# Optimization experiments

Measured on AMD Instinct MI355X. Metric: run time of the kernel, lower is better.

The kernel has to match this reference:

```python
import jax, jax.numpy as jnp
import numpy as np

B, H, W, C = 32, 56, 56, 256
WS, SHIFT, HEADS = 7, 3, 8
HD = C // HEADS
HIDDEN = 4 * C
N = WS * WS
NW = (H // WS) * (W // WS)
EPS = 1e-5


def _rel_pos_indices():
    coords = np.stack(np.meshgrid(np.arange(WS), np.arange(WS), indexing='ij'), -1).reshape(-1, 2)
    rel = coords[None, :, :] - coords[:, None, :]
    rel[..., 0] += WS - 1
    rel[..., 1] += WS - 1
    rel[..., 0] *= 2 * WS - 1
    return rel.sum(-1)  # (N, N) int

_REL_IDX = jnp.asarray(_rel_pos_indices())


def _attn_mask():
    img = np.zeros((H, W), np.float32)
    sl = (slice(0, -WS), slice(-WS, -SHIFT), slice(-SHIFT, None))
    tag = 0
    for hs in sl:
        for ws_ in sl:
            img[hs, ws_] = tag
            tag += 1
    mw = img.reshape(H // WS, WS, W // WS, WS).transpose(0, 2, 1, 3).reshape(-1, N)
    diff = mw[:, None, :] - mw[:, :, None]
    return jnp.asarray(np.where(diff != 0, -100.0, 0.0).astype(np.float32))  # (NW, N, N)

_MASK = _attn_mask()


def _layernorm(x, g, b):
    mu = x.mean(-1, keepdims=True)
    var = ((x - mu) ** 2).mean(-1, keepdims=True)
    return (x - mu) * jax.lax.rsqrt(var + EPS) * g + b


def _win_partition(x):  # (B,H,W,C) -> (B*NW, N, C)
    x = x.reshape(B, H // WS, WS, W // WS, WS, C)
    return x.transpose(0, 1, 3, 2, 4, 5).reshape(-1, N, C)


def _win_reverse(w):  # (B*NW, N, C) -> (B,H,W,C)
    x = w.reshape(B, H // WS, W // WS, WS, WS, C)
    return x.transpose(0, 1, 3, 2, 4, 5).reshape(B, H, W, C)


def setup_inputs() -> dict:
    key = jax.random.key(0)
    ks = jax.random.split(key, 16)
    s = 0.02
    return {
        'x': jax.random.normal(ks[0], (B, H * W, C), jnp.float32),
        'norm1_g': jnp.ones((C,), jnp.float32),
        'norm1_b': jnp.zeros((C,), jnp.float32),
        'qkv_w': jax.random.normal(ks[1], (C, 3 * C), jnp.float32) * s,
        'qkv_b': jnp.zeros((3 * C,), jnp.float32),
        'rel_bias': jax.random.normal(ks[2], ((2 * WS - 1) ** 2, HEADS), jnp.float32) * s,
        'proj_w': jax.random.normal(ks[3], (C, C), jnp.float32) * s,
        'proj_b': jnp.zeros((C,), jnp.float32),
        'norm2_g': jnp.ones((C,), jnp.float32),
        'norm2_b': jnp.zeros((C,), jnp.float32),
        'fc1_w': jax.random.normal(ks[4], (C, HIDDEN), jnp.float32) * s,
        'fc1_b': jnp.zeros((HIDDEN,), jnp.float32),
        'fc2_w': jax.random.normal(ks[5], (HIDDEN, C), jnp.float32) * s,
        'fc2_b': jnp.zeros((C,), jnp.float32),
    }


def reference(x, norm1_g, norm1_b, qkv_w, qkv_b, rel_bias, proj_w, proj_b,
              norm2_g, norm2_b, fc1_w, fc1_b, fc2_w, fc2_b):
    shortcut = x
    h = _layernorm(x, norm1_g, norm1_b).reshape(B, H, W, C)
    h = jnp.roll(h, (-SHIFT, -SHIFT), axis=(1, 2))
    xw = _win_partition(h)  # (B*NW, N, C)

    qkv = xw @ qkv_w + qkv_b  # (B*NW, N, 3C)
    qkv = qkv.reshape(-1, N, 3, HEADS, HD).transpose(2, 0, 3, 1, 4)
    q, k, v = qkv[0], qkv[1], qkv[2]  # (B*NW, HEADS, N, HD)
    q = q * (HD ** -0.5)
    attn = jnp.einsum('whnd,whmd->whnm', q, k)  # (B*NW, HEADS, N, N)

    bias = rel_bias[_REL_IDX].transpose(2, 0, 1)  # (HEADS, N, N)
    attn = attn + bias[None]
    attn = attn.reshape(B, NW, HEADS, N, N) + _MASK[None, :, None]
    attn = jax.nn.softmax(attn.reshape(-1, HEADS, N, N), axis=-1)

    out = jnp.einsum('whnm,whmd->whnd', attn, v)  # (B*NW, HEADS, N, HD)
    out = out.transpose(0, 2, 1, 3).reshape(-1, N, C)
    out = out @ proj_w + proj_b

    h = _win_reverse(out)
    h = jnp.roll(h, (SHIFT, SHIFT), axis=(1, 2)).reshape(B, H * W, C)

    x = shortcut + h
    m = _layernorm(x, norm2_g, norm2_b)
    m = jax.nn.gelu(m @ fc1_w + fc1_b, approximate=False) @ fc2_w + fc2_b
    return x + m
```

## Files before the change

kernel.cpp:

```cpp
#include <hip/hip_runtime.h>
#include <math.h>

static constexpr long T_TOK = 100352;

typedef __attribute__((ext_vector_type(8))) short short8;
typedef __attribute__((ext_vector_type(8))) unsigned short ushort8v;
typedef __attribute__((ext_vector_type(4))) float floatx4;

__device__ __forceinline__ float b2f(unsigned short u) {
    return __uint_as_float(((unsigned)u) << 16);
}
__device__ __forceinline__ unsigned short f2b(float f) {
    unsigned u = __float_as_uint(f);
    u += 0x7FFFu + ((u >> 16) & 1u);
    return (unsigned short)(u >> 16);
}

__device__ __forceinline__ void gload_lds16(const unsigned short* g, unsigned short* l) {
    __builtin_amdgcn_global_load_lds(
        (const __attribute__((address_space(1))) void*)g,
        (__attribute__((address_space(3))) void*)l, 16, 0, 0);
}

__global__ void detect_kernel(const unsigned short* __restrict__ x, int* flag) {
    __shared__ int cnt;
    if (threadIdx.x == 0) cnt = 0;
    __syncthreads();
    int local = 0;
    for (int i = 0; i < 16; ++i) {
        float a = fabsf(b2f(x[threadIdx.x * 16 + i]));
        if (a >= 0.015625f && a <= 8.0f) local++;
    }
    atomicAdd(&cnt, local);
    __syncthreads();
    if (threadIdx.x == 0) *flag = (cnt < 3072) ? 1 : 0;
}

__global__ void conv_kernel(const void* __restrict__ src, unsigned short* __restrict__ dst,
                            int n, const int* __restrict__ flag) {
    int i = blockIdx.x * 256 + threadIdx.x;
    if (i >= n) return;
    if (*flag) dst[i] = f2b(((const float*)src)[i]);
    else       dst[i] = ((const unsigned short*)src)[i];
}

__global__ void convT_kernel(const void* __restrict__ src, unsigned short* __restrict__ dst,
                             int K, int N, const int* __restrict__ flag) {
    int i = blockIdx.x * 256 + threadIdx.x;
    if (i >= K * N) return;
    int k = i / N, n = i - k * N;
    unsigned short v = (*flag) ? f2b(((const float*)src)[i])
                               : ((const unsigned short*)src)[i];
    dst[(long)n * K + k] = v;
}

__global__ __launch_bounds__(256) void ln_kernel(
    const void* __restrict__ xin,
    const unsigned short* __restrict__ g,
    const unsigned short* __restrict__ bsh,
    unsigned short* __restrict__ out, int mode, const int* __restrict__ flagp)
{
    int lane = threadIdx.x & 63;
    int wv = threadIdx.x >> 6;
    long t = (long)blockIdx.x * 4 + wv;
    int c0 = lane * 4;
    bool f32 = flagp && (*flagp != 0);
    float v0, v1, v2, v3;
    if (f32) {
        float4 xv = *(const float4*)((const float*)xin + t * 256 + c0);
        v0 = xv.x; v1 = xv.y; v2 = xv.z; v3 = xv.w;
    } else {
        ushort4 xv = *(const ushort4*)((const unsigned short*)xin + t * 256 + c0);
        v0 = b2f(xv.x); v1 = b2f(xv.y); v2 = b2f(xv.z); v3 = b2f(xv.w);
    }
    float s1 = v0 + v1 + v2 + v3;
    float s2 = v0*v0 + v1*v1 + v2*v2 + v3*v3;
    #pragma unroll
    for (int off = 32; off > 0; off >>= 1) {
        s1 += __shfl_down(s1, off, 64);
        s2 += __shfl_down(s2, off, 64);
    }
    s1 = __shfl(s1, 0, 64);
    s2 = __shfl(s2, 0, 64);
    float mean = s1 * (1.0f / 256.0f);
    float var  = s2 * (1.0f / 256.0f) - mean * mean;
    float rs = rsqrtf(fmaxf(var, 0.0f) + 1e-5f);
    ushort4 gv = *(const ushort4*)(g + c0);
    ushort4 bv = *(const ushort4*)(bsh + c0);
    ushort4 ov;
    ov.x = f2b((v0 - mean) * rs * b2f(gv.x) + b2f(bv.x));
    ov.y = f2b((v1 - mean) * rs * b2f(gv.y) + b2f(bv.y));
    ov.z = f2b((v2 - mean) * rs * b2f(gv.z) + b2f(bv.z));
    ov.w = f2b((v3 - mean) * rs * b2f(gv.w) + b2f(bv.w));
    long oidx;
    if (mode == 0) {
        int b_ = (int)(t / 3136);
        int hw = (int)(t % 3136);
        int hh = hw / 56, wc = hw % 56;
        int i = hh - 3; if (i < 0) i += 56;
        int j = wc - 3; if (j < 0) j += 56;
        oidx = ((long)(b_ * 64 + (i / 7) * 8 + (j / 7)) * 49
                + (i % 7) * 7 + (j % 7)) * 256 + c0;
    } else {
        oidx = t * 256 + c0;
    }
    *(ushort4*)(out + oidx) = ov;
}

__global__ __launch_bounds__(256) void gemm_mfma(
    const unsigned short* __restrict__ A,
    const unsigned short* __restrict__ Bt,
    const unsigned short* __restrict__ bias,
    void* __restrict__ out,
    const void* __restrict__ res,
    int M, int N, int K, int mode,
    const int* __restrict__ resflag, const int* __restrict__ oflag)
{
    __shared__ __align__(16) unsigned short As[128][32];
    __shared__ __align__(16) unsigned short Bs[128][32];
    const int tid  = threadIdx.x;
    const int lane = tid & 63, wave = tid >> 6;
    const int q = lane >> 4, l16 = lane & 15;
    const int wm = wave >> 1, wn = wave & 1;
    const long m0 = (long)blockIdx.y * 128;
    const int  n0 = blockIdx.x * 128;

    const int srow  = tid >> 2;
    const int skcol = (tid & 3) * 8;

    floatx4 acc[4][4];
    #pragma unroll
    for (int i = 0; i < 4; ++i)
        #pragma unroll
        for (int j = 0; j < 4; ++j)
            acc[i][j] = (floatx4){0.f, 0.f, 0.f, 0.f};

    const unsigned short* Ag = A  + (m0 + srow) * (long)K + skcol;
    const unsigned short* Bg = Bt + ((long)(n0 + srow)) * K + skcol;
    unsigned short* AsL = &As[0][0] + (long)wave * 512;
    unsigned short* BsL = &Bs[0][0] + (long)wave * 512;
    const long rowK64 = 64 * (long)K;

    for (int k0 = 0; k0 < K; k0 += 32) {
        __syncthreads();
        gload_lds16(Ag + k0,          AsL);
        gload_lds16(Ag + k0 + rowK64, AsL + 2048);
        gload_lds16(Bg + k0,          BsL);
        gload_lds16(Bg + k0 + rowK64, BsL + 2048);
        __syncthreads();
        short8 af[4], bfr[4];
        #pragma unroll
        for (int i = 0; i < 4; ++i)
            af[i] = *(const short8*)&As[wm * 64 + i * 16 + l16][q * 8];
        #pragma unroll
        for (int j = 0; j < 4; ++j)
            bfr[j] = *(const short8*)&Bs[wn * 64 + j * 16 + l16][q * 8];
        #pragma unroll
        for (int i = 0; i < 4; ++i)
            #pragma unroll
            for (int j = 0; j < 4; ++j)
                acc[i][j] = __builtin_amdgcn_mfma_f32_16x16x32_bf16(
                    af[i], bfr[j], acc[i][j], 0, 0, 0);
    }

    const bool resf32 = resflag && (*resflag != 0);
    const bool outf32 = oflag && (*oflag != 0);
    unsigned short* outb = (unsigned short*)out;
    float* outf = (float*)out;
    #pragma unroll
    for (int i = 0; i < 4; ++i) {
        #pragma unroll
        for (int r = 0; r < 4; ++r) {
            long grow = m0 + wm * 64 + i * 16 + q * 4 + r;
            long natRow = 0;
            if (mode == 1) {
                int w = (int)(grow / 49), n = (int)(grow % 49);
                int b_ = w >> 6, widx = w & 63;
                int wi = widx >> 3, wj = widx & 7;
                int pi = n / 7, pj = n % 7;
                int ii = wi * 7 + pi, jj = wj * 7 + pj;
                int h = ii + 3; if (h >= 56) h -= 56;
                int wc = jj + 3; if (wc >= 56) wc -= 56;
                natRow = ((long)b_ * 3136 + h * 56 + wc);
            }
            #pragma unroll
            for (int j = 0; j < 4; ++j) {
                int gcol = n0 + wn * 64 + j * 16 + l16;
                float v = acc[i][j][r] + b2f(bias[gcol]);
                if (mode == 2) {
                    v = 0.5f * v * (1.0f + erff(v * 0.70710678118654752f));
                    outb[grow * N + gcol] = f2b(v);
                } else if (mode == 0) {
                    outb[grow * N + gcol] = f2b(v);
                } else if (mode == 3) {
                    long o = grow * N + gcol;
                    float rv = outf32 ? outf[o] : b2f(((const unsigned short*)res)[o]);
                    v += rv;
                    if (outf32) outf[o] = v; else outb[o] = f2b(v);
                } else {
                    long o = natRow * 256 + gcol;
                    float rv = resf32 ? ((const float*)res)[o]
                                      : b2f(((const unsigned short*)res)[o]);
                    v += rv;
                    if (outf32) outf[o] = v; else outb[o] = f2b(v);
                }
            }
        }
    }
}

__global__ __launch_bounds__(256) void attn_mfma(
    const unsigned short* __restrict__ qkv,
    const unsigned short* __restrict__ rel_bias,
    unsigned short* __restrict__ out)
{
    __shared__ __align__(16) unsigned short bias_s[1360];
    __shared__ __align__(16) unsigned short Vt[4][32][72];
    __shared__ __align__(16) unsigned short Ps[4][64][72];
    const int tid = threadIdx.x;
    const int lane = tid & 63, wave = tid >> 6;
    const int q = lane >> 4, l16 = lane & 15;
    const int unit = blockIdx.x * 4 + wave;
    const int w = unit >> 3, h = unit & 7;
    const int widx = w & 63, wi = widx >> 3, wj = widx & 7;

    for (int e = tid; e < 1352; e += 256) bias_s[e] = rel_bias[e];

    const long vbase = (long)w * 49 * 768 + 512 + h * 32;
    #pragma unroll 4
    for (int it = 0; it < 32; ++it) {
        int idx = it * 64 + lane;
        int key = idx >> 5, d = idx & 31;
        unsigned short v = (key < 49) ? qkv[vbase + (long)key * 768 + d]
                                      : (unsigned short)0;
        Vt[wave][d][key] = v;
    }
    __syncthreads();

    const long qbase = (long)w * 49 * 768 + h * 32;
    short8 qf[4], kf[4];
    #pragma unroll
    for (int i = 0; i < 4; ++i) {
        int qr = l16 + 16 * i; if (qr > 48) qr = 48;
        qf[i] = *(const short8*)(qkv + qbase + (long)qr * 768 + q * 8);
    }
    #pragma unroll
    for (int j = 0; j < 4; ++j) {
        int kr = l16 + 16 * j; if (kr > 48) kr = 48;
        kf[j] = *(const short8*)(qkv + qbase + 256 + (long)kr * 768 + q * 8);
    }

    floatx4 sc[4][4];
    #pragma unroll
    for (int i = 0; i < 4; ++i)
        #pragma unroll
        for (int j = 0; j < 4; ++j)
            sc[i][j] = __builtin_amdgcn_mfma_f32_16x16x32_bf16(
                qf[i], kf[j], (floatx4){0.f, 0.f, 0.f, 0.f}, 0, 0, 0);

    int imj[4], jmj[4], tmj[4], validj[4];
    #pragma unroll
    for (int j = 0; j < 4; ++j) {
        int key = 16 * j + l16;
        validj[j] = key < 49;
        int k2 = validj[j] ? key : 48;
        int im = k2 / 7, jm = k2 - im * 7;
        imj[j] = im; jmj[j] = jm;
        int rm = wi * 7 + im, cm = wj * 7 + jm;
        tmj[j] = (rm < 49 ? 0 : (rm < 53 ? 1 : 2)) * 3
               + (cm < 49 ? 0 : (cm < 53 ? 1 : 2));
    }

    const float scale = 0.17677669529663687f;
    #pragma unroll
    for (int i = 0; i < 4; ++i) {
        #pragma unroll
        for (int r = 0; r < 4; ++r) {
            int query = 16 * i + 4 * q + r;
            int qn = query > 48 ? 48 : query;
            int in_ = qn / 7, jn = qn - in_ * 7;
            int rn = wi * 7 + in_, cn = wj * 7 + jn;
            int tn = (rn < 49 ? 0 : (rn < 53 ? 1 : 2)) * 3
                   + (cn < 49 ? 0 : (cn < 53 ? 1 : 2));
            float sv[4];
            float mx = -1e30f;
            #pragma unroll
            for (int j = 0; j < 4; ++j) {
                float s = sc[i][j][r] * scale;
                int ridx = (imj[j] - in_ + 6) * 13 + (jmj[j] - jn + 6);
                s += b2f(bias_s[ridx * 8 + h]);
                if (tmj[j] != tn) s -= 100.0f;
                if (!validj[j]) s = -1e30f;
                sv[j] = s;
                mx = fmaxf(mx, s);
            }
            #pragma unroll
            for (int m = 1; m < 16; m <<= 1)
                mx = fmaxf(mx, __shfl_xor(mx, m, 64));
            float sum = 0.0f;
            #pragma unroll
            for (int j = 0; j < 4; ++j) { sv[j] = __expf(sv[j] - mx); sum += sv[j]; }
            #pragma unroll
            for (int m = 1; m < 16; m <<= 1)
                sum += __shfl_xor(sum, m, 64);
            float inv = 1.0f / sum;
            #pragma unroll
            for (int j = 0; j < 4; ++j)
                Ps[wave][query][16 * j + l16] = f2b(sv[j] * inv);
        }
    }

    floatx4 oacc[4][2];
    #pragma unroll
    for (int i = 0; i < 4; ++i)
        #pragma unroll
        for (int jd = 0; jd < 2; ++jd)
            oacc[i][jd] = (floatx4){0.f, 0.f, 0.f, 0.f};
    #pragma unroll
    for (int s = 0; s < 2; ++s) {
        short8 vfr[2];
        #pragma unroll
        for (int jd = 0; jd < 2; ++jd)
            vfr[jd] = *(const short8*)&Vt[wave][l16 + 16 * jd][32 * s + q * 8];
        #pragma unroll
        for (int i = 0; i < 4; ++i) {
            short8 pfr = *(const short8*)&Ps[wave][l16 + 16 * i][32 * s + q * 8];
            #pragma unroll
            for (int jd = 0; jd < 2; ++jd)
                oacc[i][jd] = __builtin_amdgcn_mfma_f32_16x16x32_bf16(
                    pfr, vfr[jd], oacc[i][jd], 0, 0, 0);
        }
    }

    const long obase = (long)w * 49 * 256 + h * 32;
    #pragma unroll
    for (int i = 0; i < 4; ++i) {
        #pragma unroll
        for (int r = 0; r < 4; ++r) {
            int query = 16 * i + 4 * q + r;
            if (query < 49) {
                #pragma unroll
                for (int jd = 0; jd < 2; ++jd)
                    out[obase + (long)query * 256 + 16 * jd + l16] =
                        f2b(oacc[i][jd][r]);
            }
        }
    }
}

extern "C" void kernel_launch(void* const* d_in, const int* in_sizes, int n_in,
                              void* d_out, int out_size, void* d_ws, size_t ws_size,
                              hipStream_t stream) {
    (void)n_in; (void)out_size; (void)ws_size; (void)in_sizes;
    unsigned short* ws  = (unsigned short*)d_ws;
    const size_t TT = (size_t)T_TOK;

    unsigned short* r0  = ws;
    unsigned short* r1  = ws + TT * 256;
    unsigned short* pb  = ws + TT * 256 + TT * 1024;
    const size_t O_QKVW = 0,      O_QKVB = 196608, O_RELB = 197376, O_PROJW = 198728;
    const size_t O_PROJB = 264264, O_N1G = 264520, O_N1B = 264776;
    const size_t O_N2G = 265032,  O_N2B = 265288, O_FC1W = 265544, O_FC1B = 527688;
    const size_t O_FC2W = 528712, O_FC2B = 790856, O_PEND = 791112;
    int* flag = (int*)(pb + O_PEND);

    detect_kernel<<<1, 256, 0, stream>>>((const unsigned short*)d_in[0], flag);

    struct { int idx; size_t off; int n; } cv[9] = {
        {1, O_N1G, 256}, {2, O_N1B, 256}, {4, O_QKVB, 768},
        {5, O_RELB, 1352}, {7, O_PROJB, 256},
        {8, O_N2G, 256}, {9, O_N2B, 256}, {11, O_FC1B, 1024}, {13, O_FC2B, 256},
    };
    for (int i = 0; i < 9; ++i)
        conv_kernel<<<(cv[i].n + 255) / 256, 256, 0, stream>>>(
            d_in[cv[i].idx], pb + cv[i].off, cv[i].n, flag);
    convT_kernel<<<(196608 + 255) / 256, 256, 0, stream>>>(d_in[3],  pb + O_QKVW, 256, 768,  flag);
    convT_kernel<<<(65536  + 255) / 256, 256, 0, stream>>>(d_in[6],  pb + O_PROJW, 256, 256, flag);
    convT_kernel<<<(262144 + 255) / 256, 256, 0, stream>>>(d_in[10], pb + O_FC1W, 256, 1024, flag);
    convT_kernel<<<(262144 + 255) / 256, 256, 0, stream>>>(d_in[12], pb + O_FC2W, 1024, 256, flag);

    const long T = T_TOK;
    unsigned short* xw       = r0;
    unsigned short* qkv      = r1;
    unsigned short* attn_out = r0;
    unsigned short* x2n      = r0;
    unsigned short* hidden   = r1;

    ln_kernel<<<dim3(T / 4), 256, 0, stream>>>(d_in[0], pb + O_N1G, pb + O_N1B, xw, 0, flag);
    gemm_mfma<<<dim3(6, T / 128), 256, 0, stream>>>(xw, pb + O_QKVW, pb + O_QKVB, qkv,
                                                    nullptr, (int)T, 768, 256, 0,
                                                    nullptr, nullptr);
    attn_mfma<<<dim3(4096), 256, 0, stream>>>(qkv, pb + O_RELB, attn_out);
    gemm_mfma<<<dim3(2, T / 128), 256, 0, stream>>>(attn_out, pb + O_PROJW, pb + O_PROJB,
                                                    d_out, d_in[0], (int)T, 256, 256, 1,
                                                    flag, flag);
    ln_kernel<<<dim3(T / 4), 256, 0, stream>>>(d_out, pb + O_N2G, pb + O_N2B, x2n, 1, flag);
    gemm_mfma<<<dim3(8, T / 128), 256, 0, stream>>>(x2n, pb + O_FC1W, pb + O_FC1B, hidden,
                                                    nullptr, (int)T, 1024, 256, 2,
                                                    nullptr, nullptr);
    gemm_mfma<<<dim3(2, T / 128), 256, 0, stream>>>(hidden, pb + O_FC2W, pb + O_FC2B, d_out,
                                                    d_out, (int)T, 256, 1024, 3,
                                                    nullptr, flag);
}
```

Baseline: 1.068 ms.

## Double-buffer GEMM LDS tiles and remap workgroups across XCDs

The MFMA GEMM now uses two LDS buffers. The next K-tile's global-to-LDS loads are issued before the current tile's MFMAs run, and only one barrier is used per iteration instead of two. Block indices are also remapped so that workgroups placed round-robin on the eight XCDs get contiguous tile ranges, which should improve L2 locality. This doubles LDS use per block, and the remap assumes the total block count divides evenly by 8.

Measured after the change: 1.066 ms. About the same (-0.2%).

```diff
diff --git a/kernel.cpp b/kernel.cpp
--- a/kernel.cpp
+++ b/kernel.cpp
@@ -116,14 +116,21 @@
     int M, int N, int K, int mode,
     const int* __restrict__ resflag, const int* __restrict__ oflag)
 {
-    __shared__ __align__(16) unsigned short As[128][32];
-    __shared__ __align__(16) unsigned short Bs[128][32];
+    __shared__ __align__(16) unsigned short lds[2][8192];
     const int tid  = threadIdx.x;
     const int lane = tid & 63, wave = tid >> 6;
     const int q = lane >> 4, l16 = lane & 15;
     const int wm = wave >> 1, wn = wave & 1;
-    const long m0 = (long)blockIdx.y * 128;
-    const int  n0 = blockIdx.x * 128;
+
+    const int gx  = (int)gridDim.x;
+    const int nwg = gx * (int)gridDim.y;
+    const int lin = (int)blockIdx.y * gx + (int)blockIdx.x;
+    const int chunk = nwg >> 3;
+    const int lin2 = (lin & 7) * chunk + (lin >> 3);
+    const int bx = lin2 % gx, by = lin2 / gx;
+
+    const long m0 = (long)by * 128;
+    const int  n0 = bx * 128;
 
     const int srow  = tid >> 2;
     const int skcol = (tid & 3) * 8;
@@ -137,31 +144,40 @@
 
     const unsigned short* Ag = A  + (m0 + srow) * (long)K + skcol;
     const unsigned short* Bg = Bt + ((long)(n0 + srow)) * K + skcol;
-    unsigned short* AsL = &As[0][0] + (long)wave * 512;
-    unsigned short* BsL = &Bs[0][0] + (long)wave * 512;
     const long rowK64 = 64 * (long)K;
-
-    for (int k0 = 0; k0 < K; k0 += 32) {
-        __syncthreads();
-        gload_lds16(Ag + k0,          AsL);
-        gload_lds16(Ag + k0 + rowK64, AsL + 2048);
-        gload_lds16(Bg + k0,          BsL);
-        gload_lds16(Bg + k0 + rowK64, BsL + 2048);
-        __syncthreads();
+    const int  wbase  = wave * 512;
+
+#define STAGE(b, k0) do {                                      \
+        unsigned short* Lb = &lds[(b)][wbase];                 \
+        gload_lds16(Ag + (k0),          Lb);                   \
+        gload_lds16(Ag + (k0) + rowK64, Lb + 2048);            \
+        gload_lds16(Bg + (k0),          Lb + 4096);            \
+        gload_lds16(Bg + (k0) + rowK64, Lb + 6144);            \
+    } while (0)
+
+    const int nt = K >> 5;
+    STAGE(0, 0);
+    __syncthreads();
+    int cur = 0;
+    for (int t = 0; t < nt; ++t) {
+        if (t + 1 < nt) STAGE(cur ^ 1, (t + 1) << 5);
         short8 af[4], bfr[4];
         #pragma unroll
         for (int i = 0; i < 4; ++i)
-            af[i] = *(const short8*)&As[wm * 64 + i * 16 + l16][q * 8];
+            af[i] = *(const short8*)&lds[cur][(wm * 64 + i * 16 + l16) * 32 + q * 8];
         #pragma unroll
         for (int j = 0; j < 4; ++j)
-            bfr[j] = *(const short8*)&Bs[wn * 64 + j * 16 + l16][q * 8];
+            bfr[j] = *(const short8*)&lds[cur][4096 + (wn * 64 + j * 16 + l16) * 32 + q * 8];
         #pragma unroll
         for (int i = 0; i < 4; ++i)
             #pragma unroll
             for (int j = 0; j < 4; ++j)
                 acc[i][j] = __builtin_amdgcn_mfma_f32_16x16x32_bf16(
                     af[i], bfr[j], acc[i][j], 0, 0, 0);
-    }
+        __syncthreads();
+        cur ^= 1;
+    }
+#undef STAGE
 
     const bool resf32 = resflag && (*resflag != 0);
     const bool outf32 = oflag && (*oflag != 0);
```

## Replace LDS-staged GEMM tiles with direct register loads and double buffering

Applied to the files above, without the earlier changes.

The GEMM no longer stages A and B tiles through shared memory with global_load_lds and two barriers per k-step. Each wave now loads its MFMA fragments straight from global memory into registers, using a two-stage register double buffer over 64-wide k chunks so loads overlap the MFMAs. This removes the barriers and LDS traffic, but tiles shared by the two waves along each dimension are now fetched from global/L2 twice, and each lane's 16-byte reads are strided by K.

After: 1.453 ms. +36.1%, slower.

```diff
diff --git a/kernel.cpp b/kernel.cpp
--- a/kernel.cpp
+++ b/kernel.cpp
@@ -14,12 +14,6 @@
     unsigned u = __float_as_uint(f);
     u += 0x7FFFu + ((u >> 16) & 1u);
     return (unsigned short)(u >> 16);
-}
-
-__device__ __forceinline__ void gload_lds16(const unsigned short* g, unsigned short* l) {
-    __builtin_amdgcn_global_load_lds(
-        (const __attribute__((address_space(1))) void*)g,
-        (__attribute__((address_space(3))) void*)l, 16, 0, 0);
 }
 
 __global__ void detect_kernel(const unsigned short* __restrict__ x, int* flag) {
@@ -116,8 +110,6 @@
     int M, int N, int K, int mode,
     const int* __restrict__ resflag, const int* __restrict__ oflag)
 {
-    __shared__ __align__(16) unsigned short As[128][32];
-    __shared__ __align__(16) unsigned short Bs[128][32];
     const int tid  = threadIdx.x;
     const int lane = tid & 63, wave = tid >> 6;
     const int q = lane >> 4, l16 = lane & 15;
@@ -125,9 +117,6 @@
     const long m0 = (long)blockIdx.y * 128;
     const int  n0 = blockIdx.x * 128;
 
-    const int srow  = tid >> 2;
-    const int skcol = (tid & 3) * 8;
-
     floatx4 acc[4][4];
     #pragma unroll
     for (int i = 0; i < 4; ++i)
@@ -135,32 +124,45 @@
         for (int j = 0; j < 4; ++j)
             acc[i][j] = (floatx4){0.f, 0.f, 0.f, 0.f};
 
-    const unsigned short* Ag = A  + (m0 + srow) * (long)K + skcol;
-    const unsigned short* Bg = Bt + ((long)(n0 + srow)) * K + skcol;
-    unsigned short* AsL = &As[0][0] + (long)wave * 512;
-    unsigned short* BsL = &Bs[0][0] + (long)wave * 512;
-    const long rowK64 = 64 * (long)K;
-
-    for (int k0 = 0; k0 < K; k0 += 32) {
-        __syncthreads();
-        gload_lds16(Ag + k0,          AsL);
-        gload_lds16(Ag + k0 + rowK64, AsL + 2048);
-        gload_lds16(Bg + k0,          BsL);
-        gload_lds16(Bg + k0 + rowK64, BsL + 2048);
-        __syncthreads();
-        short8 af[4], bfr[4];
-        #pragma unroll
-        for (int i = 0; i < 4; ++i)
-            af[i] = *(const short8*)&As[wm * 64 + i * 16 + l16][q * 8];
-        #pragma unroll
-        for (int j = 0; j < 4; ++j)
-            bfr[j] = *(const short8*)&Bs[wn * 64 + j * 16 + l16][q * 8];
+    const unsigned short* Ap[4];
+    const unsigned short* Bp[4];
+    #pragma unroll
+    for (int i = 0; i < 4; ++i)
+        Ap[i] = A + (m0 + wm * 64 + i * 16 + l16) * (long)K + q * 8;
+    #pragma unroll
+    for (int j = 0; j < 4; ++j)
+        Bp[j] = Bt + (long)(n0 + wn * 64 + j * 16 + l16) * K + q * 8;
+
+    short8 a0[4], b0[4], a1[4], b1[4];
+    #pragma unroll
+    for (int i = 0; i < 4; ++i) a0[i] = *(const short8*)(Ap[i]);
+    #pragma unroll
+    for (int j = 0; j < 4; ++j) b0[j] = *(const short8*)(Bp[j]);
+
+    #pragma unroll 1
+    for (int k0 = 0; k0 < K; k0 += 64) {
+        #pragma unroll
+        for (int i = 0; i < 4; ++i) a1[i] = *(const short8*)(Ap[i] + k0 + 32);
+        #pragma unroll
+        for (int j = 0; j < 4; ++j) b1[j] = *(const short8*)(Bp[j] + k0 + 32);
         #pragma unroll
         for (int i = 0; i < 4; ++i)
             #pragma unroll
             for (int j = 0; j < 4; ++j)
                 acc[i][j] = __builtin_amdgcn_mfma_f32_16x16x32_bf16(
-                    af[i], bfr[j], acc[i][j], 0, 0, 0);
+                    a0[i], b0[j], acc[i][j], 0, 0, 0);
+        if (k0 + 64 < K) {
+            #pragma unroll
+            for (int i = 0; i < 4; ++i) a0[i] = *(const short8*)(Ap[i] + k0 + 64);
+            #pragma unroll
+            for (int j = 0; j < 4; ++j) b0[j] = *(const short8*)(Bp[j] + k0 + 64);
+        }
+        #pragma unroll
+        for (int i = 0; i < 4; ++i)
+            #pragma unroll
+            for (int j = 0; j < 4; ++j)
+                acc[i][j] = __builtin_amdgcn_mfma_f32_16x16x32_bf16(
+                    a1[i], b1[j], acc[i][j], 0, 0, 0);
     }
 
     const bool resf32 = resflag && (*resflag != 0);
```
